# Kernel optimization log

Hardware: AMD Instinct MI355X
Metric: run time of the kernel (lower is better)

The kernel has to match this reference:

```python
import jax, jax.numpy as jnp
import numpy as np

B = 16384
DM, DP, DV = 128, 16, 32
DMAP = DP + DV  # 48
QMAX = 127.0 / 128.0

IDX = [(0, 4, 0, 4, 0), (0, 4, 0, 4, 2), (0, 4, 3, 7, 1), (0, 4, 3, 7, -1),
       (3, 7, 3, 7, 2), (3, 7, 3, 7, 0), (3, 7, 0, 4, -1), (3, 7, 0, 4, 1)]


def mish(x):
    return x * jnp.tanh(jax.nn.softplus(x))


def fake_quant(x, scale):
    # straight-through rounding to 1/scale grid
    return x + jax.lax.stop_gradient(jnp.round(x * scale) / scale - x)


def ladder_conv(x, w, b):
    # w: [3, Cout, Cin]; builds 2x2 kernel [[w0, 0], [w1, w2]]
    co, ci = w.shape[1], w.shape[2]
    k = jnp.stack([w[0], jnp.zeros_like(w[0]), w[1], w[2]], axis=2).reshape(co, ci, 2, 2)
    y = jax.lax.conv_general_dilated(x, k, (1, 1), 'VALID',
                                     dimension_numbers=('NCHW', 'OIHW', 'NCHW'))
    return y + b[None, :, None, None]


def conv1x1_bn(x, w, b, s, t, act=True):
    h = jnp.einsum('oi,bihw->bohw', w, x) + b[None, :, None, None]
    h = h * s[None, :, None, None] + t[None, :, None, None]  # eval-mode BN folded
    return mish(h) if act else h


def reference(x, lw1, lb1, lw23, lb23, cw, cb, cs, ct, cwf, cbf, csf, ctf,
              pw1, pb1, pw2, pb2, pq, vw, vb, vw4, vb4):
    # gather the 8 rotated 4x4 corner chunks into one big batch [8B, 2, 4, 4]
    chunks = jnp.concatenate(
        [jnp.rot90(x[:, :, y0:y1, x0:x1], k, axes=(2, 3)) for y0, y1, x0, x1, k in IDX],
        axis=0)
    h = mish(ladder_conv(chunks, lw1, lb1))            # [8B, 128, 3, 3]
    h = conv1x1_bn(h, cw[0], cb[0], cs[0], ct[0])
    h = mish(ladder_conv(h, lw23[0], lb23[0]))         # [8B, 128, 2, 2]
    h = conv1x1_bn(h, cw[1], cb[1], cs[1], ct[1])
    h = mish(ladder_conv(h, lw23[1], lb23[1]))         # [8B, 128, 1, 1]
    h = conv1x1_bn(h, cw[2], cb[2], cs[2], ct[2])
    h = conv1x1_bn(h, cwf, cbf, csf, ctf, act=False)   # [8B, 48, 1, 1]
    feat = fake_quant(jnp.clip(h[:, :, 0, 0], -1.0, QMAX), 128.0)
    feat = feat.reshape(8, -1, DMAP).sum(0)            # [B, 48]

    pk = jax.nn.relu(feat[:, :DP] @ pw1.T + pb1)
    pk = pk @ pw2.T + pb2
    policy = (pk @ pq.T).reshape(-1, 7, 7)

    v = feat[:, DP:]
    for i in range(3):
        qw = fake_quant(jnp.clip(vw[i], -1.0, QMAX), 128.0)
        qb = fake_quant(vb[i], 128.0 * 128.0)
        v = jnp.clip(v, 0.0, QMAX) @ qw.T + qb
    qw = fake_quant(jnp.clip(vw4, -1.0, QMAX), 128.0)
    qb = fake_quant(vb4, 128.0 * 128.0)
    v = jnp.clip(v, 0.0, QMAX) @ qw.T + qb             # [B, 3]
    return (v, policy)


def setup_inputs():
    key = jax.random.key(0)
    ks = iter(jax.random.split(key, 32))
    n = lambda shape, sc: jax.random.normal(next(ks), shape, jnp.float32) * sc
    return {
        'x': jax.random.uniform(next(ks), (B, 2, 7, 7), jnp.float32),
        'lw1': n((3, DM, 2), 0.5), 'lb1': n((DM,), 0.05),
        'lw23': n((2, 3, DM, DM), 0.08), 'lb23': n((2, DM), 0.05),
        'cw': n((3, DM, DM), 0.08), 'cb': n((3, DM), 0.05),
        'cs': 1.0 + n((3, DM), 0.05), 'ct': n((3, DM), 0.05),
        'cwf': n((DMAP, DM), 0.08), 'cbf': n((DMAP,), 0.05),
        'csf': 1.0 + n((DMAP,), 0.05), 'ctf': n((DMAP,), 0.05),
        'pw1': n((DP, DP), 0.2), 'pb1': n((DP,), 0.05),
        'pw2': n((DP, DP), 0.2), 'pb2': n((DP,), 0.05),
        'pq': jax.random.normal(next(ks), (49, DP), jnp.float32),
        'vw': n((3, DV, DV), 0.2), 'vb': n((3, DV), 0.05),
        'vw4': n((3, DV), 0.2), 'vb4': n((3,), 0.05),
    }
```

## Files before the change

### kernel.cpp

```cpp
#include <hip/hip_runtime.h>
#include <hip/hip_bf16.h>

typedef _Float16 f16;
typedef f16 f16x2 __attribute__((ext_vector_type(2)));
typedef f16 f16x8 __attribute__((ext_vector_type(8)));
typedef float f32x4 __attribute__((ext_vector_type(4)));

#define QMAXF (127.0f/128.0f)

enum {
  OFF_W1 = 153600, OFF_B1 = 154368, OFF_CB = 154496, OFF_LB = 154880,
  OFF_FB = 155136, OFF_PW1 = 155184, OFF_PB1 = 155440, OFF_PW2 = 155456,
  OFF_PB2 = 155712, OFF_PQ = 155728, OFF_QW = 156512, OFF_QB = 159584,
  OFF_QW4 = 159680, OFF_QB4 = 159776, WS_TOTAL = 159779
};
enum {
  GW_C = 0,
  GW_L = 49152,
  GW_F = 147456,
  GW_1 = 153600,
  GW_TOTAL = 157696
};

__device__ __forceinline__ bool detect_bf16(const void* x){
  const unsigned short* u = (const unsigned short*)x;
  int hits = 0;
  #pragma unroll
  for (int i = 0; i < 32; i += 2){
    unsigned short h = u[i];
    hits += (h >= 0x3800 && h <= 0x3F80) ? 1 : 0;
  }
  return hits >= 12;
}

__device__ __forceinline__ float rd(const void* p, int i, bool bfl){
  return bfl ? __bfloat162float(((const __hip_bfloat16*)p)[i]) : ((const float*)p)[i];
}

__device__ __forceinline__ float mish_f(float x){
  float u = __expf(x);
  float m = fmaf(u, u + 2.0f, 2.0f);
  return fmaf(-2.0f*x, __builtin_amdgcn_rcpf(m), x);
}

__global__ void prep_kernel(const void* x, const void* lw1, const void* lb1, const void* lw23,
                            const void* lb23, const void* cw, const void* cb, const void* cs,
                            const void* ct, const void* cwf, const void* cbf, const void* csf,
                            const void* ctf, const void* pw1, const void* pb1, const void* pw2,
                            const void* pb2, const void* pq, const void* vw, const void* vb,
                            const void* vw4, const void* vb4, float* ws)
{
  const bool bfl = detect_bf16(x);
  f16* wf = (f16*)ws;
  const int t0 = blockIdx.x*blockDim.x + threadIdx.x;
  const int stride = gridDim.x*blockDim.x;

  for (int e = t0; e < GW_TOTAL; e += stride){
    float w;
    if (e < GW_L){
      int l = e >> 14, r = e & 16383;
      int kseg = r >> 10, col = (r >> 3) & 127, j = r & 7, k = kseg*8 + j;
      w = rd(cw, (l*128 + col)*128 + k, bfl) * rd(cs, l*128 + col, bfl);
    } else if (e < GW_F){
      int ee = e - GW_L;
      int lt = ee >> 14, r = ee & 16383;
      int kseg = r >> 10, col = (r >> 3) & 127, j = r & 7, k = kseg*8 + j;
      w = rd(lw23, lt*16384 + col*128 + k, bfl);
    } else if (e < GW_1){
      int ee = e - GW_F;
      int kseg = ee / 384, r = ee % 384, col = r >> 3, j = r & 7, k = kseg*8 + j;
      w = rd(cwf, col*128 + k, bfl) * rd(csf, col, bfl);
    } else {
      int ee = e - GW_1;
      int kseg = ee >> 10, col = (ee >> 3) & 127, j = ee & 7;
      w = (kseg == 0 && j < 6) ? rd(lw1, ((j>>1)*128 + col)*2 + (j&1), bfl) : 0.0f;
    }
    wf[e] = (f16)w;
  }

  for (int i = t0; i < 6179; i += stride){
    float v; int s = i;
    if (s < 768){ int tap = s>>8, r = s&255, c = r>>7, o = r&127; v = rd(lw1,(tap*128+o)*2+c,bfl); }
    else if (s < 896){ v = rd(lb1, s-768, bfl); }
    else if (s < 1280){ int idx = s-896; v = rd(cb,idx,bfl)*rd(cs,idx,bfl)+rd(ct,idx,bfl); }
    else if (s < 1536){ v = rd(lb23, s-1280, bfl); }
    else if (s < 1584){ int m = s-1536; v = rd(cbf,m,bfl)*rd(csf,m,bfl)+rd(ctf,m,bfl); }
    else if (s < 1840){ v = rd(pw1, s-1584, bfl); }
    else if (s < 1856){ v = rd(pb1, s-1840, bfl); }
    else if (s < 2112){ v = rd(pw2, s-1856, bfl); }
    else if (s < 2128){ v = rd(pb2, s-2112, bfl); }
    else if (s < 2912){ v = rd(pq, s-2128, bfl); }
    else if (s < 5984){ float w = rd(vw, s-2912, bfl); w = fminf(fmaxf(w,-1.f),QMAXF); v = rintf(w*128.f)*0.0078125f; }
    else if (s < 6080){ v = rintf(rd(vb, s-5984, bfl)*16384.f)*6.103515625e-05f; }
    else if (s < 6176){ float w = rd(vw4, s-6080, bfl); w = fminf(fmaxf(w,-1.f),QMAXF); v = rintf(w*128.f)*0.0078125f; }
    else { v = rintf(rd(vb4, s-6176, bfl)*16384.f)*6.103515625e-05f; }
    ws[153600 + i] = v;
  }
}

template<int LMAP>
__device__ __forceinline__ int map_row2(int ro, int tap){
  if (LMAP == 0) return ro;
  if (LMAP == 1){
    int smp = ro >> 5, w = ro & 31, g = w >> 2, p = w & 3;
    return smp*72 + g*9 + (p>>1)*3 + (p&1) + (tap==0 ? 0 : (tap==1 ? 3 : 4));
  }
  int smp = ro >> 3, g = ro & 7;
  return smp*32 + g*4 + (tap==0 ? 0 : (tap==1 ? 2 : 3));
}


template<int MTILES, int MSRC, int MDST, int TAPS, int LMAP>
__device__ __forceinline__ void mfma_layer(const f16* __restrict__ wf, int wbase,
                                           const float* __restrict__ ws, int boff,
                                           const f16* src, f16* dst, int lane, int wv)
{
  const int lr = lane & 15;
  const int lk = lane >> 4;
  const int c0 = wv*16 + lr;
  constexpr int SS = MSRC + 2;
  constexpr int SD = MDST + 2;

  const f16* srck = src + lk*SS*8;
  f16* dstw = dst + ((c0>>3)*SD + lk*4)*8 + (c0&7);

  f32x4 acc[MTILES];
  const float bb = ws[boff + c0];
  #pragma unroll
  for (int mt = 0; mt < MTILES; ++mt) acc[mt] = (f32x4){bb, bb, bb, bb};

  #pragma unroll
  for (int tap = 0; tap < TAPS; ++tap){
    int rowoff[MTILES];
    #pragma unroll
    for (int mt = 0; mt < MTILES; ++mt)
      rowoff[mt] = map_row2<LMAP>(mt*16 + lr, tap) * 8;

    const f16* whk = wf + wbase + tap*16384 + (lk*128 + c0)*8;

    #pragma unroll
    for (int s = 0; s < 4; ++s){
      f16x8 bh = *(const f16x8*)(whk + s*4096);
      #pragma unroll
      for (int mt = 0; mt < MTILES; ++mt){
        f16x8 ah = *(const f16x8*)(srck + s*4*SS*8 + rowoff[mt]);
        acc[mt] = __builtin_amdgcn_mfma_f32_16x16x32_f16(ah, bh, acc[mt], 0, 0, 0);
      }
    }
  }

  #pragma unroll
  for (int mt = 0; mt < MTILES; ++mt)
    #pragma unroll
    for (int r = 0; r < 4; ++r)
      dstw[(mt*16 + r)*8] = (f16)mish_f(acc[mt][r]);
}

__global__ __launch_bounds__(512, 4)
void fused_kernel(const void* __restrict__ xv, const float* __restrict__ ws, void* __restrict__ outv)
{
  __shared__ __align__(16) f16 bufA[18688];
  __shared__ __align__(16) f16 bufB[18688];

  float* xraw = (float*)bufB;
  f16*   a1   = bufB + 400;
  float* qbuf = (float*)bufA;
  float* featL= (float*)bufA + 768;
  float* pkA  = (float*)bufA + 864;
  float* pkB  = (float*)bufA + 896;
  float* vA   = (float*)bufA + 928;
  float* vB   = (float*)bufA + 992;
  float* vC   = (float*)bufA + 1056;

  const int tid  = threadIdx.x;
  const int lane = tid & 63;
  const int wv   = tid >> 6;
  const int b    = blockIdx.x;
  const bool bfl = detect_bf16(xv);
  const f16* wf  = (const f16*)ws;

  if (tid < 196){
    int smp = tid >= 98 ? 1 : 0;
    int q = tid - 98*smp;
    xraw[smp*98 + q] = rd(xv, (b*2 + smp)*98 + q, bfl);
  }
  __syncthreads();

  for (int e2 = tid; e2 < 576; e2 += 512){
    const int row = e2 >> 2, kh = e2 & 3;
    f16x2 hv = (f16x2){(f16)0.f, (f16)0.f};
    if (kh < 3){
      const int smp = row >= 72 ? 1 : 0;
      const int rr = row - 72*smp;
      const int g = (rr*57) >> 9;
      const int q = rr - 9*g;
      const int i = (q*11) >> 5;
      const int j = q - 3*i;
      const int ri = i + (kh >= 1), rj = j + (kh == 2);
      const int kk = (0x13023120u >> (g*4)) & 0xF;
      const int y0 = (g >= 4) ? 3 : 0;
      const int x0 = (g >= 2 && g <= 5) ? 3 : 0;
      int sy, sx;
      if      (kk == 0){ sy = ri;     sx = rj;     }
      else if (kk == 1){ sy = rj;     sx = 3 - ri; }
      else if (kk == 2){ sy = 3 - ri; sx = 3 - rj; }
      else             { sy = 3 - rj; sx = ri;     }
      const int base = smp*98 + (y0 + sy)*7 + (x0 + sx);
      hv[0] = (f16)xraw[base];
      hv[1] = (f16)xraw[base + 49];
    }
    *(f16x2*)(a1 + row*8 + kh*2) = hv;
  }
  __syncthreads();

  {
    const int lr = lane & 15, lk = lane >> 4;
    const int c0 = wv*16 + lr;
    const f16x8 bh = *(const f16x8*)(wf + GW_1 + (lk*128 + c0)*8);
    const float bb = ws[OFF_B1 + c0];
    f16* dstw = bufA + ((c0>>3)*146 + lk*4)*8 + (c0&7);
    f32x4 acc[9];
    #pragma unroll
    for (int mt = 0; mt < 9; ++mt) acc[mt] = (f32x4){bb, bb, bb, bb};
    #pragma unroll
    for (int mt = 0; mt < 9; ++mt){
      f16x8 ah = *(const f16x8*)(a1 + (mt*16 + lr)*8);
      acc[mt] = __builtin_amdgcn_mfma_f32_16x16x32_f16(ah, bh, acc[mt], 0, 0, 0);
    }
    #pragma unroll
    for (int mt = 0; mt < 9; ++mt)
      #pragma unroll
      for (int r = 0; r < 4; ++r)
        dstw[(mt*16 + r)*8] = (f16)mish_f(acc[mt][r]);
  }
  __syncthreads();

  mfma_layer<9,144,144,1,0>(wf, GW_C,          ws, OFF_CB,       bufA, bufB, lane, wv);
  __syncthreads();
  mfma_layer<4,144, 64,3,1>(wf, GW_L,          ws, OFF_LB,       bufB, bufA, lane, wv);
  __syncthreads();
  mfma_layer<4, 64, 64,1,0>(wf, GW_C + 16384,  ws, OFF_CB + 128, bufA, bufB, lane, wv);
  __syncthreads();
  mfma_layer<1, 64, 16,3,2>(wf, GW_L + 49152,  ws, OFF_LB + 128, bufB, bufA, lane, wv);
  __syncthreads();
  mfma_layer<1, 16, 16,1,0>(wf, GW_C + 32768,  ws, OFF_CB + 256, bufA, bufB, lane, wv);
  __syncthreads();

  if (wv < 3){
    const int lr = lane & 15, lk = lane >> 4;
    const int col = wv*16 + lr;
    const float bb = ws[OFF_FB + col];
    const f16* srck = bufB + lk*18*8 + lr*8;
    f32x4 a1acc = (f32x4){bb, bb, bb, bb};
    #pragma unroll
    for (int s = 0; s < 4; ++s){
      f16x8 af = *(const f16x8*)(srck + s*4*18*8);
      f16x8 bh = *(const f16x8*)(wf + GW_F + ((4*s + lk)*48 + col)*8);
      a1acc = __builtin_amdgcn_mfma_f32_16x16x32_f16(af, bh, a1acc, 0, 0, 0);
    }
    #pragma unroll
    for (int r = 0; r < 4; ++r){
      const int row = lk*4 + r;
      float h = fminf(fmaxf(a1acc[r], -1.0f), QMAXF);
      qbuf[row*48 + col] = rintf(h * 128.0f) * 0.0078125f;
    }
  }
  __syncthreads();

  if (wv < 4){
    const int hsmp = wv & 1;
    const int bi = b*2 + hsmp;
    if (wv < 2){
      if (lane < 16){
        float f = 0.f;
        #pragma unroll
        for (int g = 0; g < 8; ++g) f += qbuf[(hsmp*8 + g)*48 + lane];
        featL[hsmp*48 + lane] = f;
      }
      if (lane < 16){
        float a = ws[OFF_PB1 + lane];
        #pragma unroll
        for (int c = 0; c < 16; ++c) a = fmaf(featL[hsmp*48 + c], ws[OFF_PW1 + lane*16 + c], a);
        pkA[hsmp*16 + lane] = fmaxf(a, 0.0f);
      }
      if (lane < 16){
        float a = ws[OFF_PB2 + lane];
        #pragma unroll
        for (int c = 0; c < 16; ++c) a = fmaf(pkA[hsmp*16 + c], ws[OFF_PW2 + lane*16 + c], a);
        pkB[hsmp*16 + lane] = a;
      }
      if (lane < 49){
        float a = 0.0f;
        #pragma unroll
        for (int c = 0; c < 16; ++c) a = fmaf(pkB[hsmp*16 + c], ws[OFF_PQ + lane*16 + c], a);
        const int idx = 49152 + bi*49 + lane;
        if (bfl) ((__hip_bfloat16*)outv)[idx] = __float2bfloat16(a);
        else     ((float*)outv)[idx] = a;
      }
    } else {
      if (lane < 32){
        float f = 0.f;
        #pragma unroll
        for (int g = 0; g < 8; ++g) f += qbuf[(hsmp*8 + g)*48 + 16 + lane];
        featL[hsmp*48 + 16 + lane] = f;
      }
      if (lane < 32){
        float a = ws[OFF_QB + lane];
        #pragma unroll
        for (int c = 0; c < 32; ++c)
          a = fmaf(fminf(fmaxf(featL[hsmp*48 + 16 + c], 0.0f), QMAXF), ws[OFF_QW + lane*32 + c], a);
        vA[hsmp*32 + lane] = a;
      }
      if (lane < 32){
        float a = ws[OFF_QB + 32 + lane];
        #pragma unroll
        for (int c = 0; c < 32; ++c)
          a = fmaf(fminf(fmaxf(vA[hsmp*32 + c], 0.0f), QMAXF), ws[OFF_QW + 1024 + lane*32 + c], a);
        vB[hsmp*32 + lane] = a;
      }
      if (lane < 32){
        float a = ws[OFF_QB + 64 + lane];
        #pragma unroll
        for (int c = 0; c < 32; ++c)
          a = fmaf(fminf(fmaxf(vB[hsmp*32 + c], 0.0f), QMAXF), ws[OFF_QW + 2048 + lane*32 + c], a);
        vC[hsmp*32 + lane] = a;
      }
      if (lane < 3){
        float a = ws[OFF_QB4 + lane];
        #pragma unroll
        for (int c = 0; c < 32; ++c)
          a = fmaf(fminf(fmaxf(vC[hsmp*32 + c], 0.0f), QMAXF), ws[OFF_QW4 + lane*32 + c], a);
        const int idx = bi*3 + lane;
        if (bfl) ((__hip_bfloat16*)outv)[idx] = __float2bfloat16(a);
        else     ((float*)outv)[idx] = a;
      }
    }
  }
}

extern "C" void kernel_launch(void* const* d_in, const int* in_sizes, int n_in,
                              void* d_out, int out_size, void* d_ws, size_t ws_size,
                              hipStream_t stream)
{
  (void)in_sizes; (void)n_in; (void)out_size; (void)ws_size;
  float* ws = (float*)d_ws;
  prep_kernel<<<256, 256, 0, stream>>>(
      d_in[0],  d_in[1],  d_in[2],  d_in[3],  d_in[4],  d_in[5],  d_in[6],  d_in[7],
      d_in[8],  d_in[9],  d_in[10], d_in[11], d_in[12], d_in[13], d_in[14], d_in[15],
      d_in[16], d_in[17], d_in[18], d_in[19], d_in[20], d_in[21], ws);
  fused_kernel<<<8192, 512, 0, stream>>>(d_in[0], ws, d_out);
}
```

Baseline: 269.3 us.

## Run MFMA layers in place on one shared buffer to raise occupancy

New measurement: 257.3 us. 1.05x faster.

```diff
diff --git a/kernel.cpp b/kernel.cpp
--- a/kernel.cpp
+++ b/kernel.cpp
@@ -109,20 +109,19 @@
   return smp*32 + g*4 + (tap==0 ? 0 : (tap==1 ? 2 : 3));
 }
 
-
-template<int MTILES, int MSRC, int MDST, int TAPS, int LMAP>
-__device__ __forceinline__ void mfma_layer(const f16* __restrict__ wf, int wbase,
-                                           const float* __restrict__ ws, int boff,
-                                           const f16* src, f16* dst, int lane, int wv)
+#define BS 146
+
+template<int MTILES, int ROW0, int TAPS, int LMAP>
+__device__ __forceinline__ void layer_ip(const f16* __restrict__ wf, int wbase,
+                                         const float* __restrict__ ws, int boff,
+                                         f16* buf, int lane, int wv)
 {
   const int lr = lane & 15;
   const int lk = lane >> 4;
   const int c0 = wv*16 + lr;
-  constexpr int SS = MSRC + 2;
-  constexpr int SD = MDST + 2;
-
-  const f16* srck = src + lk*SS*8;
-  f16* dstw = dst + ((c0>>3)*SD + lk*4)*8 + (c0&7);
+
+  const f16* srck = buf + lk*BS*8;
+  f16* dstw = buf + ((c0>>3)*BS + ROW0 + lk*4)*8 + (c0&7);
 
   f32x4 acc[MTILES];
   const float bb = ws[boff + c0];
@@ -134,7 +133,7 @@
     int rowoff[MTILES];
     #pragma unroll
     for (int mt = 0; mt < MTILES; ++mt)
-      rowoff[mt] = map_row2<LMAP>(mt*16 + lr, tap) * 8;
+      rowoff[mt] = map_row2<LMAP>(ROW0 + mt*16 + lr, tap) * 8;
 
     const f16* whk = wf + wbase + tap*16384 + (lk*128 + c0)*8;
 
@@ -143,11 +142,13 @@
       f16x8 bh = *(const f16x8*)(whk + s*4096);
       #pragma unroll
       for (int mt = 0; mt < MTILES; ++mt){
-        f16x8 ah = *(const f16x8*)(srck + s*4*SS*8 + rowoff[mt]);
+        f16x8 ah = *(const f16x8*)(srck + s*4*BS*8 + rowoff[mt]);
         acc[mt] = __builtin_amdgcn_mfma_f32_16x16x32_f16(ah, bh, acc[mt], 0, 0, 0);
       }
     }
   }
+
+  __syncthreads();
 
   #pragma unroll
   for (int mt = 0; mt < MTILES; ++mt)
@@ -156,21 +157,20 @@
       dstw[(mt*16 + r)*8] = (f16)mish_f(acc[mt][r]);
 }
 
-__global__ __launch_bounds__(512, 4)
+__global__ __launch_bounds__(512, 6)
 void fused_kernel(const void* __restrict__ xv, const float* __restrict__ ws, void* __restrict__ outv)
 {
-  __shared__ __align__(16) f16 bufA[18688];
-  __shared__ __align__(16) f16 bufB[18688];
-
-  float* xraw = (float*)bufB;
-  f16*   a1   = bufB + 400;
-  float* qbuf = (float*)bufA;
-  float* featL= (float*)bufA + 768;
-  float* pkA  = (float*)bufA + 864;
-  float* pkB  = (float*)bufA + 896;
-  float* vA   = (float*)bufA + 928;
-  float* vB   = (float*)bufA + 992;
-  float* vC   = (float*)bufA + 1056;
+  __shared__ __align__(16) f16 buf[16*BS*8];
+  __shared__ __align__(16) float scratch[1120];
+
+  f16*   a1   = (f16*)scratch;
+  float* qbuf = scratch;
+  float* featL= scratch + 768;
+  float* pkA  = scratch + 864;
+  float* pkB  = scratch + 896;
+  float* vA   = scratch + 928;
+  float* vB   = scratch + 992;
+  float* vC   = scratch + 1056;
 
   const int tid  = threadIdx.x;
   const int lane = tid & 63;
@@ -178,13 +178,6 @@
   const int b    = blockIdx.x;
   const bool bfl = detect_bf16(xv);
   const f16* wf  = (const f16*)ws;
-
-  if (tid < 196){
-    int smp = tid >= 98 ? 1 : 0;
-    int q = tid - 98*smp;
-    xraw[smp*98 + q] = rd(xv, (b*2 + smp)*98 + q, bfl);
-  }
-  __syncthreads();
 
   for (int e2 = tid; e2 < 576; e2 += 512){
     const int row = e2 >> 2, kh = e2 & 3;
@@ -205,9 +198,9 @@
       else if (kk == 1){ sy = rj;     sx = 3 - ri; }
       else if (kk == 2){ sy = 3 - ri; sx = 3 - rj; }
       else             { sy = 3 - rj; sx = ri;     }
-      const int base = smp*98 + (y0 + sy)*7 + (x0 + sx);
-      hv[0] = (f16)xraw[base];
-      hv[1] = (f16)xraw[base + 49];
+      const int gi = (b*2 + smp)*98 + (y0 + sy)*7 + (x0 + sx);
+      hv[0] = (f16)rd(xv, gi, bfl);
+      hv[1] = (f16)rd(xv, gi + 49, bfl);
     }
     *(f16x2*)(a1 + row*8 + kh*2) = hv;
   }
@@ -218,7 +211,7 @@
     const int c0 = wv*16 + lr;
     const f16x8 bh = *(const f16x8*)(wf + GW_1 + (lk*128 + c0)*8);
     const float bb = ws[OFF_B1 + c0];
-    f16* dstw = bufA + ((c0>>3)*146 + lk*4)*8 + (c0&7);
+    f16* dstw = buf + ((c0>>3)*BS + lk*4)*8 + (c0&7);
     f32x4 acc[9];
     #pragma unroll
     for (int mt = 0; mt < 9; ++mt) acc[mt] = (f32x4){bb, bb, bb, bb};
@@ -235,33 +228,34 @@
   }
   __syncthreads();
 
-  mfma_layer<9,144,144,1,0>(wf, GW_C,          ws, OFF_CB,       bufA, bufB, lane, wv);
-  __syncthreads();
-  mfma_layer<4,144, 64,3,1>(wf, GW_L,          ws, OFF_LB,       bufB, bufA, lane, wv);
-  __syncthreads();
-  mfma_layer<4, 64, 64,1,0>(wf, GW_C + 16384,  ws, OFF_CB + 128, bufA, bufB, lane, wv);
-  __syncthreads();
-  mfma_layer<1, 64, 16,3,2>(wf, GW_L + 49152,  ws, OFF_LB + 128, bufB, bufA, lane, wv);
-  __syncthreads();
-  mfma_layer<1, 16, 16,1,0>(wf, GW_C + 32768,  ws, OFF_CB + 256, bufA, bufB, lane, wv);
+  layer_ip<5,  0, 1, 0>(wf, GW_C,         ws, OFF_CB,       buf, lane, wv);
+  layer_ip<4, 80, 1, 0>(wf, GW_C,         ws, OFF_CB,       buf, lane, wv);
+  __syncthreads();
+  layer_ip<4,  0, 3, 1>(wf, GW_L,         ws, OFF_LB,       buf, lane, wv);
+  __syncthreads();
+  layer_ip<4,  0, 1, 0>(wf, GW_C + 16384, ws, OFF_CB + 128, buf, lane, wv);
+  __syncthreads();
+  layer_ip<1,  0, 3, 2>(wf, GW_L + 49152, ws, OFF_LB + 128, buf, lane, wv);
+  __syncthreads();
+  layer_ip<1,  0, 1, 0>(wf, GW_C + 32768, ws, OFF_CB + 256, buf, lane, wv);
   __syncthreads();
 
   if (wv < 3){
     const int lr = lane & 15, lk = lane >> 4;
     const int col = wv*16 + lr;
     const float bb = ws[OFF_FB + col];
-    const f16* srck = bufB + lk*18*8 + lr*8;
-    f32x4 a1acc = (f32x4){bb, bb, bb, bb};
+    const f16* srck = buf + (lk*BS + lr)*8;
+    f32x4 fa = (f32x4){bb, bb, bb, bb};
     #pragma unroll
     for (int s = 0; s < 4; ++s){
-      f16x8 af = *(const f16x8*)(srck + s*4*18*8);
+      f16x8 af = *(const f16x8*)(srck + s*4*BS*8);
       f16x8 bh = *(const f16x8*)(wf + GW_F + ((4*s + lk)*48 + col)*8);
-      a1acc = __builtin_amdgcn_mfma_f32_16x16x32_f16(af, bh, a1acc, 0, 0, 0);
+      fa = __builtin_amdgcn_mfma_f32_16x16x32_f16(af, bh, fa, 0, 0, 0);
     }
     #pragma unroll
     for (int r = 0; r < 4; ++r){
       const int row = lk*4 + r;
-      float h = fminf(fmaxf(a1acc[r], -1.0f), QMAXF);
+      float h = fminf(fmaxf(fa[r], -1.0f), QMAXF);
       qbuf[row*48 + col] = rintf(h * 128.0f) * 0.0078125f;
     }
   }
```
